# Kernel optimization log

Hardware: AMD Instinct MI355X
Metric: run time of the kernel (lower is better)

## Reference

```python
import jax, jax.numpy as jnp
import numpy as np

M, K, N = 4096, 4096, 4096

def setup_inputs() -> dict:
    key = jax.random.key(0)
    k1, k2, k3, k4 = jax.random.split(key, 4)
    a = jax.random.randint(k1, (M, K), 0, 127, dtype=jnp.int32)  # int8 activations
    b = jax.random.randint(k2, (N, K), 0, 127, dtype=jnp.int32)  # int8 weights [N,K]
    alpha_row = jax.random.uniform(k3, (M, 1), dtype=jnp.float32)  # per-row dequant scale
    alpha_col = jax.random.uniform(k4, (1, N), dtype=jnp.float32)  # per-col dequant scale
    return {"a": a, "b": b, "alpha_row": alpha_row, "alpha_col": alpha_col}

def reference(a, b, alpha_row, alpha_col):
    # x = a_fp32 @ b_fp32^T  -> [M, N]
    x = jnp.matmul(a.astype(jnp.float32), b.astype(jnp.float32).T)
    # outer-product dequant scale [M,1] x [1,N] -> [M,N], fused multiply
    out = x * (alpha_row * alpha_col)
    return out.astype(jnp.float16)
```

## Files before the change

### kernel.cpp

```cpp
#include <hip/hip_runtime.h>


constexpr int MD = 4096, ND = 4096, KD = 4096;
constexpr int BM = 256, BN = 256, BKB = 128;
constexpr int NT = KD / BKB;
constexpr int TB = BM * BKB;

using i32x4 = __attribute__((ext_vector_type(4))) int;

#define VMCNT(n) asm volatile("s_waitcnt vmcnt(" #n ")" ::: "memory")
#define BAR() __builtin_amdgcn_s_barrier()
#define FENCE() __builtin_amdgcn_sched_barrier(0)

__global__ __launch_bounds__(256) void pack_i8(const int* __restrict__ in,
                                               char* __restrict__ out) {
  const size_t t = (size_t)blockIdx.x * 256 + threadIdx.x;
  const int4* p = (const int4*)in + t * 4;
  int4 v0 = p[0], v1 = p[1], v2 = p[2], v3 = p[3];
  int4 o;
  o.x = v0.x | (v0.y << 8) | (v0.z << 16) | (v0.w << 24);
  o.y = v1.x | (v1.y << 8) | (v1.z << 16) | (v1.w << 24);
  o.z = v2.x | (v2.y << 8) | (v2.z << 16) | (v2.w << 24);
  o.w = v3.x | (v3.y << 8) | (v3.z << 16) | (v3.w << 24);
  ((int4*)out)[t] = o;
}

__device__ inline void load16_lds(const char* g, char* l) {
  __builtin_amdgcn_global_load_lds(
      (const __attribute__((address_space(1))) void*)g,
      (__attribute__((address_space(3))) void*)l, 16, 0, 0);
}

__device__ inline float f16_sat(float v) {
  v = fminf(v, 65504.0f);
  return (float)(_Float16)v;
}

__global__ __launch_bounds__(512, 2) void gemm_i8w8(
    const char* __restrict__ A, const char* __restrict__ B,
    const float* __restrict__ arow, const float* __restrict__ acol,
    float* __restrict__ out) {
  __shared__ char sA[2][TB];
  __shared__ char sB[2][TB];

  const int tid = threadIdx.x;
  const int wv = tid >> 6;
  const int lane = tid & 63;

  const int bid = blockIdx.x;
  const int wg = (bid & 7) * 32 + (bid >> 3);
  const int brow = wg >> 4;
  const int bcol = wg & 15;

  const int wrow = (wv >> 2) * 128;
  const int wcol = (wv & 3) * 64;

  i32x4 acc[8][4] = {};

  const int lr = lane >> 3;
  const int lsg = ((lane & 7) ^ lr) * 16;
  const int q0 = wv * 2, q1 = wv * 2 + 1;
  const int rA0 = (q0 >> 3) * 128 + (q0 & 7) * 8;
  const int rA1 = (q1 >> 3) * 128 + (q1 & 7) * 8;
  const int rB0 = (q0 >> 2) * 64 + (q0 & 3) * 8;
  const int rB1 = (q1 >> 2) * 64 + (q1 & 3) * 8;
  const char* srcA0 = A + (size_t)(brow * BM + rA0 + lr) * KD + lsg;
  const char* srcA1 = A + (size_t)(brow * BM + rA1 + lr) * KD + lsg;
  const char* srcB0 = B + (size_t)(bcol * BN + rB0 + lr) * KD + lsg;
  const char* srcB1 = B + (size_t)(bcol * BN + rB1 + lr) * KD + lsg;
  const size_t skip32 = (size_t)32 * KD, skip64 = (size_t)64 * KD;

  auto STAGE_ALL = [&](int nb, size_t kb) {
    load16_lds(srcA0 + kb, sA[nb] + rA0 * BKB);
    load16_lds(srcA1 + kb, sA[nb] + rA1 * BKB);
    load16_lds(srcB0 + kb, sB[nb] + rB0 * BKB);
    load16_lds(srcB1 + kb, sB[nb] + rB1 * BKB);
    load16_lds(srcB0 + skip32 + kb, sB[nb] + (rB0 + 32) * BKB);
    load16_lds(srcB1 + skip32 + kb, sB[nb] + (rB1 + 32) * BKB);
    load16_lds(srcA0 + skip64 + kb, sA[nb] + (rA0 + 64) * BKB);
    load16_lds(srcA1 + skip64 + kb, sA[nb] + (rA1 + 64) * BKB);
  };

  const int r = lane & 15;
  const int s0 = (((lane >> 4) + 0) ^ (r & 7)) * 16;
  const int s1 = (((lane >> 4) + 4) ^ (r & 7)) * 16;
  const int aBase = (wrow + r) * BKB;
  const int bBase = (wcol + r) * BKB;

  i32x4 afX[4], afY[4], bfP[2], bfQ[2];

  auto RD_A = [&](i32x4(&af)[4], const char* buf, int mh, int ks) {
    const char* p = buf + aBase + mh * 8192 + (ks ? s1 : s0);
#pragma unroll
    for (int mt = 0; mt < 4; ++mt) af[mt] = *(const i32x4*)(p + mt * 2048);
  };
  auto RD_B = [&](i32x4(&bf)[2], const char* buf, int nh, int ks) {
    const char* p = buf + bBase + nh * 4096 + (ks ? s1 : s0);
#pragma unroll
    for (int nt = 0; nt < 2; ++nt) bf[nt] = *(const i32x4*)(p + nt * 2048);
  };
  auto CLUSTER = [&](i32x4(&af)[4], i32x4(&bf)[2], int mh, int nh) {
    __builtin_amdgcn_s_setprio(1);
#pragma unroll
    for (int mt = 0; mt < 4; ++mt)
#pragma unroll
      for (int nt = 0; nt < 2; ++nt)
        acc[mh * 4 + mt][nh * 2 + nt] = __builtin_amdgcn_mfma_i32_16x16x64_i8(
            af[mt], bf[nt], acc[mh * 4 + mt][nh * 2 + nt], 0, 0, 0);
    __builtin_amdgcn_s_setprio(0);
  };

  auto tile_body = [&](int i, const char* pa, const char* pb,
                       const char* pan, const char* pbn, int nb) {
    const bool more = (i + 1) < NT;
    const size_t kb = (size_t)(i + 1) * BKB;
    CLUSTER(afX, bfP, 0, 0);
    if (more) STAGE_ALL(nb, kb);
    RD_B(bfQ, pb, 1, 0);
    FENCE();
    CLUSTER(afX, bfQ, 0, 1);
    RD_A(afY, pa, 1, 0);
    FENCE();
    CLUSTER(afY, bfQ, 1, 1);
    FENCE();
    CLUSTER(afY, bfP, 1, 0);
    RD_A(afX, pa, 1, 1);
    RD_B(bfQ, pb, 0, 1);
    FENCE();
    CLUSTER(afX, bfQ, 1, 0);
    RD_B(bfP, pb, 1, 1);
    FENCE();
    CLUSTER(afX, bfP, 1, 1);
    RD_A(afY, pa, 0, 1);
    VMCNT(2);
    BAR();
    FENCE();
    CLUSTER(afY, bfP, 0, 1);
    FENCE();
    CLUSTER(afY, bfQ, 0, 0);
    if (more) {
      RD_A(afX, pan, 0, 0);
      RD_B(bfP, pbn, 0, 0);
    }
    VMCNT(0);
    BAR();
    FENCE();
  };

  STAGE_ALL(0, 0);
  VMCNT(0);
  BAR();
  RD_A(afX, sA[0], 0, 0);
  RD_B(bfP, sB[0], 0, 0);

  for (int i = 0; i < NT; i += 2) {
    tile_body(i, sA[0], sB[0], sA[1], sB[1], 1);
    tile_body(i + 1, sA[1], sB[1], sA[0], sB[0], 0);
  }

  const int orow0 = brow * BM + wrow + ((lane >> 4) << 2);
  const int ocol0 = bcol * BN + wcol + (lane & 15);
#pragma unroll
  for (int m = 0; m < 8; ++m) {
    const int rb = orow0 + m * 16;
    const float ar0 = arow[rb + 0], ar1 = arow[rb + 1];
    const float ar2 = arow[rb + 2], ar3 = arow[rb + 3];
#pragma unroll
    for (int n = 0; n < 4; ++n) {
      const int col = ocol0 + n * 16;
      const float ac = acol[col];
      out[(size_t)(rb + 0) * ND + col] = f16_sat((float)acc[m][n][0] * (ar0 * ac));
      out[(size_t)(rb + 1) * ND + col] = f16_sat((float)acc[m][n][1] * (ar1 * ac));
      out[(size_t)(rb + 2) * ND + col] = f16_sat((float)acc[m][n][2] * (ar2 * ac));
      out[(size_t)(rb + 3) * ND + col] = f16_sat((float)acc[m][n][3] * (ar3 * ac));
    }
  }
}

extern "C" void kernel_launch(void* const* d_in, const int* in_sizes, int n_in,
                              void* d_out, int out_size, void* d_ws, size_t ws_size,
                              hipStream_t stream) {
  const int* a = (const int*)d_in[0];
  const int* b = (const int*)d_in[1];
  const float* arow = (const float*)d_in[2];
  const float* acol = (const float*)d_in[3];
  float* out = (float*)d_out;

  char* pa = (char*)d_ws;
  char* pb = pa + (size_t)MD * KD;

  const int packBlocks = (int)(((size_t)MD * KD) / (16 * 256));
  pack_i8<<<packBlocks, 256, 0, stream>>>(a, pa);
  pack_i8<<<packBlocks, 256, 0, stream>>>(b, pb);

  const int grid = (MD / BM) * (ND / BN);
  gemm_i8w8<<<grid, 512, 0, stream>>>(pa, pb, arow, acol, out);
}
```

Baseline: 96.95 us.

## Load B fragments directly from global into registers, stage only A in LDS

B tiles no longer pass through shared memory. Each wave loads its B fragments straight from global memory into double-buffered registers, while A alone is staged to LDS via global_load_lds. This halves LDS footprint and LDS read traffic, and the MFMA schedule is restructured into four 16-MFMA chunks per tile. In exchange it adds redundant global B loads across waves that share columns (two row-waves per column), uncoalesced 16-byte per-lane reads strided by K, and higher register pressure from the eight-fragment B double buffer.

Result: slower. 185.3 us (+91.1%).

```diff
diff --git a/kernel.cpp b/kernel.cpp
--- a/kernel.cpp
+++ b/kernel.cpp
@@ -4,7 +4,6 @@
 constexpr int MD = 4096, ND = 4096, KD = 4096;
 constexpr int BM = 256, BN = 256, BKB = 128;
 constexpr int NT = KD / BKB;
-constexpr int TB = BM * BKB;
 
 using i32x4 = __attribute__((ext_vector_type(4))) int;
 
@@ -40,8 +39,7 @@
     const char* __restrict__ A, const char* __restrict__ B,
     const float* __restrict__ arow, const float* __restrict__ acol,
     float* __restrict__ out) {
-  __shared__ char sA[2][TB];
-  __shared__ char sB[2][TB];
+  __shared__ char sA[2][BM * BKB];
 
   const int tid = threadIdx.x;
   const int wv = tid >> 6;
@@ -62,21 +60,13 @@
   const int q0 = wv * 2, q1 = wv * 2 + 1;
   const int rA0 = (q0 >> 3) * 128 + (q0 & 7) * 8;
   const int rA1 = (q1 >> 3) * 128 + (q1 & 7) * 8;
-  const int rB0 = (q0 >> 2) * 64 + (q0 & 3) * 8;
-  const int rB1 = (q1 >> 2) * 64 + (q1 & 3) * 8;
   const char* srcA0 = A + (size_t)(brow * BM + rA0 + lr) * KD + lsg;
   const char* srcA1 = A + (size_t)(brow * BM + rA1 + lr) * KD + lsg;
-  const char* srcB0 = B + (size_t)(bcol * BN + rB0 + lr) * KD + lsg;
-  const char* srcB1 = B + (size_t)(bcol * BN + rB1 + lr) * KD + lsg;
-  const size_t skip32 = (size_t)32 * KD, skip64 = (size_t)64 * KD;
+  const size_t skip64 = (size_t)64 * KD;
 
-  auto STAGE_ALL = [&](int nb, size_t kb) {
+  auto STAGE_A = [&](int nb, size_t kb) {
     load16_lds(srcA0 + kb, sA[nb] + rA0 * BKB);
     load16_lds(srcA1 + kb, sA[nb] + rA1 * BKB);
-    load16_lds(srcB0 + kb, sB[nb] + rB0 * BKB);
-    load16_lds(srcB1 + kb, sB[nb] + rB1 * BKB);
-    load16_lds(srcB0 + skip32 + kb, sB[nb] + (rB0 + 32) * BKB);
-    load16_lds(srcB1 + skip32 + kb, sB[nb] + (rB1 + 32) * BKB);
     load16_lds(srcA0 + skip64 + kb, sA[nb] + (rA0 + 64) * BKB);
     load16_lds(srcA1 + skip64 + kb, sA[nb] + (rA1 + 64) * BKB);
   };
@@ -85,77 +75,75 @@
   const int s0 = (((lane >> 4) + 0) ^ (r & 7)) * 16;
   const int s1 = (((lane >> 4) + 4) ^ (r & 7)) * 16;
   const int aBase = (wrow + r) * BKB;
-  const int bBase = (wcol + r) * BKB;
 
-  i32x4 afX[4], afY[4], bfP[2], bfQ[2];
+  const char* bP[4];
+#pragma unroll
+  for (int n = 0; n < 4; ++n)
+    bP[n] = B + (size_t)(bcol * BN + wcol + n * 16 + r) * KD + (lane >> 4) * 16;
 
-  auto RD_A = [&](i32x4(&af)[4], const char* buf, int mh, int ks) {
-    const char* p = buf + aBase + mh * 8192 + (ks ? s1 : s0);
+  i32x4 afX[4], afY[4], bfU[4][2], bfV[4][2];
+
+#define RDCHUNK(dst, ks, mh)                                              \
+  {                                                                       \
+    const char* p_ = sA[cb] + aBase + (mh)*8192 + ((ks) ? s1 : s0);       \
+    _Pragma("unroll") for (int j = 0; j < 4; ++j) dst[j] =                \
+        *(const i32x4*)(p_ + j * 2048);                                   \
+  }
+#define MFMA16(af, bf, ks, mh)                                            \
+  {                                                                       \
+    __builtin_amdgcn_s_setprio(1);                                        \
+    _Pragma("unroll") for (int j = 0; j < 4; ++j)                         \
+        _Pragma("unroll") for (int n = 0; n < 4; ++n) acc[(mh)*4 + j][n] =\
+        __builtin_amdgcn_mfma_i32_16x16x64_i8(af[j], bf[n][ks],           \
+                                              acc[(mh)*4 + j][n], 0, 0, 0);\
+    __builtin_amdgcn_s_setprio(0);                                        \
+  }
+
 #pragma unroll
-    for (int mt = 0; mt < 4; ++mt) af[mt] = *(const i32x4*)(p + mt * 2048);
-  };
-  auto RD_B = [&](i32x4(&bf)[2], const char* buf, int nh, int ks) {
-    const char* p = buf + bBase + nh * 4096 + (ks ? s1 : s0);
+  for (int n = 0; n < 4; ++n) {
+    bfU[n][0] = *(const i32x4*)(bP[n] + 0);
+    bfU[n][1] = *(const i32x4*)(bP[n] + 64);
+  }
+  STAGE_A(0, 0);
+  VMCNT(0);
+  BAR();
+
+  auto tile = [&](int i, int cb_, int nb, i32x4(&bfC)[4][2],
+                  i32x4(&bfN)[4][2]) {
+    const int cb = cb_;
+    const bool more = (i + 1) < NT;
+    const size_t kb = (size_t)(i + 1) * BKB;
+    if (more) {
 #pragma unroll
-    for (int nt = 0; nt < 2; ++nt) bf[nt] = *(const i32x4*)(p + nt * 2048);
-  };
-  auto CLUSTER = [&](i32x4(&af)[4], i32x4(&bf)[2], int mh, int nh) {
-    __builtin_amdgcn_s_setprio(1);
+      for (int n = 0; n < 4; ++n)
+        bfN[n][0] = *(const i32x4*)(bP[n] + kb);
+      FENCE();
+      STAGE_A(nb, kb);
+    }
+    FENCE();
+    RDCHUNK(afX, 0, 0);
+    RDCHUNK(afY, 0, 1);
+    MFMA16(afX, bfC, 0, 0);
+    if (more) {
 #pragma unroll
-    for (int mt = 0; mt < 4; ++mt)
-#pragma unroll
-      for (int nt = 0; nt < 2; ++nt)
-        acc[mh * 4 + mt][nh * 2 + nt] = __builtin_amdgcn_mfma_i32_16x16x64_i8(
-            af[mt], bf[nt], acc[mh * 4 + mt][nh * 2 + nt], 0, 0, 0);
-    __builtin_amdgcn_s_setprio(0);
+      for (int n = 0; n < 4; ++n)
+        bfN[n][1] = *(const i32x4*)(bP[n] + kb + 64);
+    }
+    FENCE();
+    RDCHUNK(afX, 1, 0);
+    MFMA16(afY, bfC, 0, 1);
+    FENCE();
+    RDCHUNK(afY, 1, 1);
+    MFMA16(afX, bfC, 1, 0);
+    FENCE();
+    MFMA16(afY, bfC, 1, 1);
+    VMCNT(0);
+    BAR();
   };
 
-  auto tile_body = [&](int i, const char* pa, const char* pb,
-                       const char* pan, const char* pbn, int nb) {
-    const bool more = (i + 1) < NT;
-    const size_t kb = (size_t)(i + 1) * BKB;
-    CLUSTER(afX, bfP, 0, 0);
-    if (more) STAGE_ALL(nb, kb);
-    RD_B(bfQ, pb, 1, 0);
-    FENCE();
-    CLUSTER(afX, bfQ, 0, 1);
-    RD_A(afY, pa, 1, 0);
-    FENCE();
-    CLUSTER(afY, bfQ, 1, 1);
-    FENCE();
-    CLUSTER(afY, bfP, 1, 0);
-    RD_A(afX, pa, 1, 1);
-    RD_B(bfQ, pb, 0, 1);
-    FENCE();
-    CLUSTER(afX, bfQ, 1, 0);
-    RD_B(bfP, pb, 1, 1);
-    FENCE();
-    CLUSTER(afX, bfP, 1, 1);
-    RD_A(afY, pa, 0, 1);
-    VMCNT(2);
-    BAR();
-    FENCE();
-    CLUSTER(afY, bfP, 0, 1);
-    FENCE();
-    CLUSTER(afY, bfQ, 0, 0);
-    if (more) {
-      RD_A(afX, pan, 0, 0);
-      RD_B(bfP, pbn, 0, 0);
-    }
-    VMCNT(0);
-    BAR();
-    FENCE();
-  };
-
-  STAGE_ALL(0, 0);
-  VMCNT(0);
-  BAR();
-  RD_A(afX, sA[0], 0, 0);
-  RD_B(bfP, sB[0], 0, 0);
-
   for (int i = 0; i < NT; i += 2) {
-    tile_body(i, sA[0], sB[0], sA[1], sB[1], 1);
-    tile_body(i + 1, sA[1], sB[1], sA[0], sB[0], 0);
+    tile(i, 0, 1, bfU, bfV);
+    tile(i + 1, 1, 0, bfV, bfU);
   }
 
   const int orow0 = brow * BM + wrow + ((lane >> 4) << 2);
```
